# Kernel tuning notes

Hardware: AMD Instinct MI355X
Metric: run time of the kernel (lower is better)

## Reference

```python
import jax, jax.numpy as jnp
import numpy as np

EMB = 768
HEADS = 12
HD = EMB // HEADS          # 64
WS = 14                    # window size
MLP = 4 * EMB
SCALE = HD ** -0.5

# relative-position lookup indices (q_size == k_size == WS)
_REL_IDX = np.arange(WS)[:, None] - np.arange(WS)[None, :] + (WS - 1)  # (WS, WS)


def setup_inputs() -> dict:
    key = jax.random.key(0)
    ks = jax.random.split(key, 12)
    w = lambda k, shape: jax.random.normal(k, shape, jnp.float32) * 0.02
    return {
        "x": jax.random.normal(ks[0], (4, 64, 64, EMB), jnp.float32),
        "clstoken": jax.random.normal(ks[1], (4, 1, EMB), jnp.float32),
        "qkv_w": w(ks[2], (EMB, 3 * EMB)),
        "qkv_b": jnp.zeros((3 * EMB,), jnp.float32),
        "proj_w": w(ks[3], (EMB, EMB)),
        "proj_b": jnp.zeros((EMB,), jnp.float32),
        "rel_pos_h": w(ks[4], (2 * WS - 1, HD)),
        "rel_pos_w": w(ks[5], (2 * WS - 1, HD)),
        "norm1_s": jnp.ones((EMB,), jnp.float32),
        "norm1_b": jnp.zeros((EMB,), jnp.float32),
        "norm2_s": jnp.ones((EMB,), jnp.float32),
        "norm2_b": jnp.zeros((EMB,), jnp.float32),
        "fc1_w": w(ks[6], (EMB, MLP)),
        "fc1_b": jnp.zeros((MLP,), jnp.float32),
        "fc2_w": w(ks[7], (MLP, EMB)),
        "fc2_b": jnp.zeros((EMB,), jnp.float32),
    }


def _layernorm(x, s, b, eps=1e-6):
    mu = jnp.mean(x, axis=-1, keepdims=True)
    var = jnp.mean(jnp.square(x - mu), axis=-1, keepdims=True)
    return (x - mu) * jax.lax.rsqrt(var + eps) * s + b


def _attn_with_clstoken(xw, cls, qkv_w, qkv_b, proj_w, proj_b, rel_pos_h, rel_pos_w):
    # xw: (Bw, WS, WS, C), cls: (Bw, 1, C)
    Bw = xw.shape[0]
    NP = WS * WS                                   # patch tokens per window
    tokens = jnp.concatenate([cls, xw.reshape(Bw, NP, EMB)], axis=1)  # (Bw, T, C)
    T = NP + 1
    qkv = (tokens @ qkv_w + qkv_b).reshape(Bw, T, 3, HEADS, HD)
    q, k, v = [qkv[:, :, i].transpose(0, 2, 1, 3) for i in range(3)]  # (Bw, H, T, HD)
    attn = jnp.einsum("bhqd,bhkd->bhqk", q * SCALE, k)                # (Bw, H, T, T)
    # decomposed relative-position bias on the patch-patch sub-block
    Rh = rel_pos_h[_REL_IDX]                       # (WS, WS, HD)
    Rw = rel_pos_w[_REL_IDX]
    r_q = q[:, :, 1:, :].reshape(Bw, HEADS, WS, WS, HD)
    rel_h = jnp.einsum("bnhwc,hkc->bnhwk", r_q, Rh)  # (Bw, H, WS, WS, WS)
    rel_w = jnp.einsum("bnhwc,wkc->bnhwk", r_q, Rw)
    bias = (rel_h[..., :, None] + rel_w[..., None, :]).reshape(Bw, HEADS, NP, NP)
    attn = attn.at[:, :, 1:, 1:].add(bias)
    attn = jax.nn.softmax(attn, axis=-1)
    out = jnp.einsum("bhqk,bhkd->bhqd", attn, v)
    out = out.transpose(0, 2, 1, 3).reshape(Bw, T, EMB) @ proj_w + proj_b
    return out[:, 1:, :].reshape(Bw, WS, WS, EMB), out[:, :1, :]


def reference(x, clstoken, qkv_w, qkv_b, proj_w, proj_b, rel_pos_h, rel_pos_w,
              norm1_s, norm1_b, norm2_s, norm2_b, fc1_w, fc1_b, fc2_w, fc2_b):
    B, H, W, C = x.shape
    HW = H * W
    tokens = jnp.concatenate([clstoken, x.reshape(B, HW, C)], axis=1)
    shortcut = tokens
    t = _layernorm(tokens, norm1_s, norm1_b)
    cls_n = t[:, :1, :]
    xn = t[:, 1:, :].reshape(B, H, W, C)
    # window partition with padding
    pad_h = (WS - H % WS) % WS
    pad_w = (WS - W % WS) % WS
    Hp, Wp = H + pad_h, W + pad_w
    xp = jnp.pad(xn, ((0, 0), (0, pad_h), (0, pad_w), (0, 0)))
    nH, nW = Hp // WS, Wp // WS
    n_windows = nH * nW
    xw = xp.reshape(B, nH, WS, nW, WS, C).transpose(0, 1, 3, 2, 4, 5)
    xw = xw.reshape(B * n_windows, WS, WS, C)
    cls_w = jnp.repeat(cls_n, n_windows, axis=0)   # repeat_interleave over batch dim
    xw, cls_w = _attn_with_clstoken(xw, cls_w, qkv_w, qkv_b, proj_w, proj_b,
                                    rel_pos_h, rel_pos_w)
    # window unpartition
    xu = xw.reshape(B, nH, nW, WS, WS, C).transpose(0, 1, 3, 2, 4, 5)
    xu = xu.reshape(B, Hp, Wp, C)[:, :H, :W, :]
    cls_out = cls_w.reshape(B, n_windows, 1, C).mean(axis=1)
    y = jnp.concatenate([cls_out, xu.reshape(B, HW, C)], axis=1)
    tokens = shortcut + y
    h = _layernorm(tokens, norm2_s, norm2_b)
    tokens = tokens + (jax.nn.gelu(h @ fc1_w + fc1_b) @ fc2_w + fc2_b)
    return tokens  # (B, 1 + H*W, C)
```

## Files before the change

kernel.cpp:

```cpp
#include <hip/hip_runtime.h>
#include <hip/hip_bf16.h>

typedef __hip_bfloat16 bf;
typedef __bf16 bf16x8 __attribute__((ext_vector_type(8)));
typedef float f32x4 __attribute__((ext_vector_type(4)));
typedef unsigned short u16x4 __attribute__((ext_vector_type(4)));

#define DEVI __device__ __forceinline__

DEVI float b2f(bf v){ return __bfloat162float(v); }

DEVI float bfbits(unsigned short v){
  unsigned u = (unsigned)v << 16; float f; __builtin_memcpy(&f, &u, 4); return f;
}

DEVI float ldx(const void* p, size_t i, int f){
  return f ? __bfloat162float(((const bf*)p)[i]) : ((const float*)p)[i];
}

DEVI f32x4 mfma16(bf16x8 a, bf16x8 b, f32x4 c){
  return __builtin_amdgcn_mfma_f32_16x16x32_bf16(a, b, c, 0, 0, 0);
}

DEVI float gelu_t(float x){
  float u = 0.7978845608028654f * (x + 0.044715f * x * x * x);
  u = fminf(fmaxf(u, -30.f), 30.f);
  float e = __expf(2.f * u);
  return 0.5f * x * (1.f + (e - 1.f) / (e + 1.f));
}

DEVI void gload16(const bf* g, char* l){
  __builtin_amdgcn_global_load_lds((const __attribute__((address_space(1))) void*)g,
                                   (__attribute__((address_space(3))) void*)l, 16, 0, 0);
}

__global__ void detect_dtype(const void* n1s, int* flag){
  unsigned u = *(const unsigned*)n1s;
  *flag = (u == 0x3F800000u) ? 0 : 1;
}

__global__ __launch_bounds__(256) void conv_bf16(const void* src, bf* dst, int n, const int* flag){
  int f = *flag;
  int i = blockIdx.x * 256 + threadIdx.x;
  if (i < n) dst[i] = f ? ((const bf*)src)[i] : __float2bfloat16(((const float*)src)[i]);
}

__global__ __launch_bounds__(256) void transpose_w(const void* __restrict__ W, bf* __restrict__ Wt,
                                                   int K, int N, const int* flag){
  __shared__ bf tile[32][33];
  const int f = *flag;
  int n0 = blockIdx.x * 32, k0 = blockIdx.y * 32;
  int tx = threadIdx.x & 31, ty = threadIdx.x >> 5;
  #pragma unroll
  for (int i = ty; i < 32; i += 8)
    tile[i][tx] = __float2bfloat16(ldx(W, (size_t)(k0 + i) * N + n0 + tx, f));
  __syncthreads();
  #pragma unroll
  for (int i = ty; i < 32; i += 8) Wt[(size_t)(n0 + i) * K + k0 + tx] = tile[tx][i];
}

DEVI void blockreduce2(float& s, float& s2){
  #pragma unroll
  for (int off = 32; off > 0; off >>= 1){
    s  += __shfl_down(s, off);
    s2 += __shfl_down(s2, off);
  }
  __shared__ float sh[8];
  int wv = threadIdx.x >> 6;
  if ((threadIdx.x & 63) == 0){ sh[wv*2] = s; sh[wv*2+1] = s2; }
  __syncthreads();
  s  = sh[0] + sh[2] + sh[4] + sh[6];
  s2 = sh[1] + sh[3] + sh[5] + sh[7];
}

__global__ __launch_bounds__(256) void ln_window(const void* __restrict__ x, const void* __restrict__ cls,
    const bf* __restrict__ g, const bf* __restrict__ bb, bf* __restrict__ winx, int b0,
    const int* flag){
  const int f = *flag;
  int row = blockIdx.x;
  int wid_g = row / 197, p = row % 197;
  int batch = b0 + wid_g / 25;
  int wid = wid_g % 25;
  int wi = wid / 5, wj = wid % 5;
  bf* dst = winx + (size_t)row * 768;
  int tid = threadIdx.x;
  const void* src = nullptr;
  size_t base = 0;
  if (p == 0){ src = cls; base = (size_t)batch * 768; }
  else {
    int pi = (p - 1) / 14, pj = (p - 1) % 14;
    int gh = wi * 14 + pi, gw = wj * 14 + pj;
    if (gh < 64 && gw < 64){ src = x; base = ((size_t)((batch * 64 + gh) * 64 + gw)) * 768; }
  }
  if (!src){
    for (int c = tid; c < 768; c += 256) dst[c] = __float2bfloat16(0.f);
    return;
  }
  float v[3]; float s = 0.f, s2 = 0.f;
  #pragma unroll
  for (int k = 0; k < 3; k++){ v[k] = ldx(src, base + tid + k*256, f); s += v[k]; s2 += v[k]*v[k]; }
  blockreduce2(s, s2);
  float mu  = s  * (1.f/768.f);
  float var = fmaxf(s2 * (1.f/768.f) - mu*mu, 0.f);
  float rs  = rsqrtf(var + 1e-6f);
  #pragma unroll
  for (int k = 0; k < 3; k++){
    int c = tid + k*256;
    dst[c] = __float2bfloat16((v[k]-mu)*rs*b2f(g[c]) + b2f(bb[c]));
  }
}

__global__ __launch_bounds__(256) void ln_f32(const float* __restrict__ in, const bf* __restrict__ g,
    const bf* __restrict__ bb, bf* __restrict__ outb){
  size_t row = blockIdx.x;
  const float* src = in + row * 768;
  bf* dst = outb + row * 768;
  int tid = threadIdx.x;
  float v[3]; float s = 0.f, s2 = 0.f;
  #pragma unroll
  for (int k = 0; k < 3; k++){ v[k] = src[tid + k*256]; s += v[k]; s2 += v[k]*v[k]; }
  blockreduce2(s, s2);
  float mu  = s  * (1.f/768.f);
  float var = fmaxf(s2 * (1.f/768.f) - mu*mu, 0.f);
  float rs  = rsqrtf(var + 1e-6f);
  #pragma unroll
  for (int k = 0; k < 3; k++){
    int c = tid + k*256;
    dst[c] = __float2bfloat16((v[k]-mu)*rs*b2f(g[c]) + b2f(bb[c]));
  }
}

__global__ __launch_bounds__(512) void gemm128(const bf* __restrict__ A, const bf* __restrict__ Bt,
    const bf* __restrict__ bias, const float* __restrict__ res, void* __restrict__ out,
    int M, int N, int K, int flags, const int* dflag, int row_off)
{
  __shared__ __bf16 sA[2][128*64];
  __shared__ __bf16 sB[2][128*64];
  const int df = *dflag;
  const int gx = gridDim.x;
  const int nwg = gx * gridDim.y;
  const int lin = blockIdx.y * gx + blockIdx.x;
  const int q = nwg >> 3, r = nwg & 7;
  const int xcd = lin & 7, pos = lin >> 3;
  const int logical = (xcd < r ? xcd * (q + 1) : r * (q + 1) + (xcd - r) * q) + pos;
  const int m0 = (logical / gx) * 128, n0 = (logical % gx) * 128;

  const int tid = threadIdx.x, wv = tid >> 6, l = tid & 63;
  const int wm = (wv >> 2) * 64;
  const int wn = (wv & 3) * 32;
  const int li = l & 15, lk = l >> 4;
  const int xr = li & 7;

  f32x4 acc[4][2];
  #pragma unroll
  for (int i = 0; i < 4; i++)
    #pragma unroll
    for (int j = 0; j < 2; j++){ f32x4 z = {0.f,0.f,0.f,0.f}; acc[i][j] = z; }

  const int rA = tid >> 3;
  const int sl = (tid & 7) ^ (rA & 7);
  const bf* gA0 = A  + (size_t)(m0 + rA)      * K + sl * 8;
  const bf* gA1 = A  + (size_t)(m0 + 64 + rA) * K + sl * 8;
  const bf* gB0 = Bt + (size_t)(n0 + rA)      * K + sl * 8;
  const bf* gB1 = Bt + (size_t)(n0 + 64 + rA) * K + sl * 8;
  const int ldsbase = wv * 1024;

  const int nt = K >> 6;
  {
    gload16(gA0, (char*)sA[0] + ldsbase);
    gload16(gA1, (char*)sA[0] + 8192 + ldsbase);
    gload16(gB0, (char*)sB[0] + ldsbase);
    gload16(gB1, (char*)sB[0] + 8192 + ldsbase);
  }
  asm volatile("s_waitcnt vmcnt(0)" ::: "memory");
  __syncthreads();

  int cur = 0;
  for (int t = 0; t < nt; t++){
    if (t + 1 < nt){
      const int ke = (t + 1) << 6;
      gload16(gA0 + ke, (char*)sA[cur^1] + ldsbase);
      gload16(gA1 + ke, (char*)sA[cur^1] + 8192 + ldsbase);
      gload16(gB0 + ke, (char*)sB[cur^1] + ldsbase);
      gload16(gB1 + ke, (char*)sB[cur^1] + 8192 + ldsbase);
    }
    const __bf16* cA = sA[cur];
    const __bf16* cB = sB[cur];
    #pragma unroll
    for (int ks = 0; ks < 2; ks++){
      const int so = ((ks*4 + lk) ^ xr) * 8;
      bf16x8 af[4], bfr[2];
      #pragma unroll
      for (int i = 0; i < 4; i++) af[i]  = *(const bf16x8*)&cA[(wm + i*16 + li)*64 + so];
      #pragma unroll
      for (int j = 0; j < 2; j++) bfr[j] = *(const bf16x8*)&cB[(wn + j*16 + li)*64 + so];
      #pragma unroll
      for (int i = 0; i < 4; i++)
        #pragma unroll
        for (int j = 0; j < 2; j++) acc[i][j] = mfma16(af[i], bfr[j], acc[i][j]);
    }
    asm volatile("s_waitcnt vmcnt(0)" ::: "memory");
    __syncthreads();
    cur ^= 1;
  }

  #pragma unroll
  for (int i = 0; i < 4; i++){
    #pragma unroll
    for (int j = 0; j < 2; j++){
      int colg = n0 + wn + j*16 + li;
      float bc = b2f(bias[colg]);
      #pragma unroll
      for (int r2 = 0; r2 < 4; r2++){
        int rowg = m0 + wm + i*16 + lk*4 + r2;
        if (rowg < M){
          float vv = acc[i][j][r2] + bc;
          if (flags & 1) vv = gelu_t(vv);
          if (flags & 2) vv += res[(size_t)rowg * N + colg];
          if (flags & 4){
            size_t oidx = (size_t)(row_off + rowg) * N + colg;
            if (df == 0) ((float*)out)[oidx] = vv;
            else         ((bf*)out)[oidx]    = __float2bfloat16(vv);
          } else {
            ((bf*)out)[(size_t)rowg * N + colg] = __float2bfloat16(vv);
          }
        }
      }
    }
  }
}

__global__ __launch_bounds__(256) void bias_tables(const bf* __restrict__ qkv,
    const bf* __restrict__ rph, const bf* __restrict__ rpw, bf* __restrict__ relT){
  const int blk = blockIdx.x;
  const int w = blk / 12, h = blk % 12;
  const int tid = threadIdx.x, wv = tid >> 6, l = tid & 63;
  const int li = l & 15, lk = l >> 4;
  const bf* qbase = qkv + (size_t)w * 197 * 2304 + h * 64;
  bf* tbase = relT + (size_t)blk * 5600;
  for (int g = wv; g < 28; g += 4){
    bool isH = (g < 14);
    int pfix = isH ? g : (g - 14);
    int var  = li < 13 ? li : 13;
    int q = isH ? (1 + pfix*14 + var) : (1 + var*14 + pfix);
    f32x4 acc = {0.f,0.f,0.f,0.f};
    const bf* rp = isH ? rph : rpw;
    #pragma unroll
    for (int s = 0; s < 2; s++){
      bf16x8 a = *(const bf16x8*)(qbase + (size_t)q * 2304 + s*32 + lk*8);
      int idx = pfix + 13 - li;
      if (idx < 0) idx = 0;
      bf16x8 b = *(const bf16x8*)(rp + idx * 64 + s*32 + lk*8);
      acc = mfma16(a, b, acc);
    }
    #pragma unroll
    for (int r = 0; r < 4; r++){
      int mrow = lk*4 + r;
      int col = li;
      if (mrow <= 13 && col <= 13){
        int qi = isH ? (pfix*14 + mrow) : (mrow*14 + pfix);
        tbase[(isH ? 0 : 2800) + col*200 + qi + 1] = __float2bfloat16(acc[r]);
      }
    }
  }
}

__global__ __launch_bounds__(256) void attn_win(const bf* __restrict__ qkv,
    const bf* __restrict__ relT, bf* __restrict__ aout){
  __shared__ __bf16 Vt[64][232];
  __shared__ __bf16 Pl[4][16][232];
  const int blk = blockIdx.x;
  const int wh = blk >> 1, half = blk & 1;
  const int w = wh / 12, h = wh % 12;
  const int tid = threadIdx.x, wv = tid >> 6, l = tid & 63;
  const int li = l & 15, lk = l >> 4;
  const bf* qp = qkv + (size_t)w * 197 * 2304 + h * 64;
  const bf* kp = qp + 768;
  const bf* vp = qp + 1536;
  {
    const int cc = (tid & 7) * 8, rb = tid >> 3;
    #pragma unroll
    for (int pass = 0; pass < 7; pass++){
      int r = pass * 32 + rb;
      __bf16 vvv[8];
      if (r < 197){
        bf16x8 t = *(const bf16x8*)(vp + (size_t)r * 2304 + cc);
        #pragma unroll
        for (int e = 0; e < 8; e++) vvv[e] = t[e];
      } else {
        #pragma unroll
        for (int e = 0; e < 8; e++) vvv[e] = (__bf16)0.f;
      }
      #pragma unroll
      for (int e = 0; e < 8; e++) Vt[cc + e][r] = vvv[e];
    }
  }
  for (int i = l; i < 256; i += 64) Pl[wv][i >> 4][208 + (i & 15)] = (__bf16)0.f;
  __syncthreads();
  const bf* rHT = relT + (size_t)wh * 5600;
  const bf* rWT = rHT + 2800;
  const int qt0 = half * 7;
  const int nqt = half ? 6 : 7;
  for (int qt_l = wv; qt_l < nqt; qt_l += 4){
    const int qt = qt0 + qt_l;
    const int grow0 = qt*16 + lk*4;
    int qrow = qt * 16 + li; if (qrow > 196) qrow = 196;
    bf16x8 qa0 = *(const bf16x8*)(qp + (size_t)qrow * 2304 + lk*8);
    bf16x8 qa1 = *(const bf16x8*)(qp + (size_t)qrow * 2304 + 32 + lk*8);
    f32x4 sc[13];
    #pragma unroll
    for (int ct = 0; ct < 13; ct++){
      int kr = ct * 16 + li; if (kr > 196) kr = 196;
      bf16x8 kb0 = *(const bf16x8*)(kp + (size_t)kr * 2304 + lk*8);
      bf16x8 kb1 = *(const bf16x8*)(kp + (size_t)kr * 2304 + 32 + lk*8);
      f32x4 z = {0.f,0.f,0.f,0.f};
      z = mfma16(qa0, kb0, z);
      z = mfma16(qa1, kb1, z);
      sc[ct] = z;
    }
    float mx[4] = {-3e38f, -3e38f, -3e38f, -3e38f};
    #pragma unroll
    for (int ct = 0; ct < 13; ct++){
      const int col = ct * 16 + li;
      const int kiq = col >= 1 ? col - 1 : 0;
      const int kh = (kiq * 4682) >> 16;
      const int kw = kiq - kh * 14;
      const u16x4 rh4 = *(const u16x4*)(rHT + kh*200 + grow0);
      const u16x4 rw4 = *(const u16x4*)(rWT + kw*200 + grow0);
      #pragma unroll
      for (int r = 0; r < 4; r++){
        int grow = grow0 + r;
        float s = sc[ct][r] * 0.125f;
        if (col >= 197) s = -1e30f;
        else if (col >= 1 && grow >= 1 && grow < 197)
          s += bfbits(rh4[r]) + bfbits(rw4[r]);
        sc[ct][r] = s;
        mx[r] = fmaxf(mx[r], s);
      }
    }
    #pragma unroll
    for (int r = 0; r < 4; r++){
      #pragma unroll
      for (int off = 1; off < 16; off <<= 1) mx[r] = fmaxf(mx[r], __shfl_xor(mx[r], off));
    }
    float den[4] = {0.f,0.f,0.f,0.f};
    #pragma unroll
    for (int ct = 0; ct < 13; ct++)
      #pragma unroll
      for (int r = 0; r < 4; r++){
        float e = __expf(sc[ct][r] - mx[r]);
        sc[ct][r] = e; den[r] += e;
      }
    #pragma unroll
    for (int r = 0; r < 4; r++){
      #pragma unroll
      for (int off = 1; off < 16; off <<= 1) den[r] += __shfl_xor(den[r], off);
      den[r] = 1.f / den[r];
    }
    #pragma unroll
    for (int ct = 0; ct < 13; ct++)
      #pragma unroll
      for (int r = 0; r < 4; r++)
        Pl[wv][lk*4 + r][ct*16 + li] = (__bf16)(sc[ct][r] * den[r]);
    asm volatile("s_waitcnt lgkmcnt(0)" ::: "memory");
    __builtin_amdgcn_sched_barrier(0);
    #pragma unroll
    for (int n = 0; n < 4; n++){
      f32x4 o = {0.f,0.f,0.f,0.f};
      #pragma unroll
      for (int ks = 0; ks < 7; ks++){
        bf16x8 pa = *(const bf16x8*)&Pl[wv][li][ks*32 + lk*8];
        bf16x8 vb = *(const bf16x8*)&Vt[n*16 + li][ks*32 + lk*8];
        o = mfma16(pa, vb, o);
      }
      #pragma unroll
      for (int r = 0; r < 4; r++){
        int grow = qt * 16 + lk*4 + r;
        if (grow < 197)
          aout[((size_t)w * 197 + grow) * 768 + h*64 + n*16 + li] = __float2bfloat16(o[r]);
      }
    }
  }
}

__global__ __launch_bounds__(256) void unwindow(const void* __restrict__ x, const void* __restrict__ cls,
    const bf* __restrict__ projoC, float* __restrict__ tok2, int b0, const int* flag){
  const int f = *flag;
  int tg = blockIdx.x;
  int bl = tg / 4097, t = tg % 4097;
  int batch = b0 + bl;
  const bf* projo = projoC + (size_t)bl * 4925 * 768;
  for (int c = threadIdx.x; c < 768; c += 256){
    float val, add;
    if (t == 0){
      val = ldx(cls, (size_t)batch * 768 + c, f);
      float s = 0.f;
      #pragma unroll
      for (int wi = 0; wi < 25; wi++)
        s += b2f(projo[((size_t)wi * 197) * 768 + c]);
      add = s * 0.04f;
    } else {
      int idx = t - 1, gh = idx >> 6, gw = idx & 63;
      int wi = gh / 14, pi = gh % 14, wj = gw / 14, pj = gw % 14;
      int wwin = wi*5 + wj, tl = 1 + pi*14 + pj;
      val = ldx(x, ((size_t)batch * 4096 + idx) * 768 + c, f);
      add = b2f(projo[((size_t)wwin * 197 + tl) * 768 + c]);
    }
    tok2[((size_t)batch * 4097 + t) * 768 + c] = val + add;
  }
}

extern "C" void kernel_launch(void* const* d_in, const int* in_sizes, int n_in,
                              void* d_out, int out_size, void* d_ws, size_t ws_size,
                              hipStream_t stream){
  (void)in_sizes; (void)n_in; (void)out_size;
  const void* x      = d_in[0];
  const void* cls    = d_in[1];
  const void* qkv_w  = d_in[2];
  const void* qkv_bv = d_in[3];
  const void* proj_w = d_in[4];
  const void* proj_bv= d_in[5];
  const void* rph    = d_in[6];
  const void* rpw    = d_in[7];
  const void* n1s    = d_in[8];
  const void* n1b    = d_in[9];
  const void* n2s    = d_in[10];
  const void* n2b    = d_in[11];
  const void* fc1_w  = d_in[12];
  const void* fc1_bv = d_in[13];
  const void* fc2_w  = d_in[14];
  const void* fc2_bv = d_in[15];

  char* ws = (char*)d_ws;
  int* flagp  = (int*)(ws + 0);
  bf* wt_qkv  = (bf*)(ws + 256);
  bf* wt_proj = (bf*)(ws + 3539200);
  bf* wt_fc1  = (bf*)(ws + 4718848);
  bf* wt_fc2  = (bf*)(ws + 9437440);
  bf* c_qkv_b = (bf*)(ws + 14156032);
  bf* c_proj_b= (bf*)(ws + 14160640);
  bf* c_fc1_b = (bf*)(ws + 14162176);
  bf* c_fc2_b = (bf*)(ws + 14168320);
  bf* c_n1s   = (bf*)(ws + 14169856);
  bf* c_n1b   = (bf*)(ws + 14171392);
  bf* c_n2s   = (bf*)(ws + 14172928);
  bf* c_n2b   = (bf*)(ws + 14174464);
  bf* c_rph   = (bf*)(ws + 14176000);
  bf* c_rpw   = (bf*)(ws + 14179456);

  const size_t base0 = 14188800;
  int nb = 1;
  if      (ws_size >= base0 + 4ull*37824000 + 50343936) nb = 4;
  else if (ws_size >= base0 + 2ull*37824000 + 50343936) nb = 2;
  const size_t o_winx  = base0;
  const size_t o_qkv   = o_winx + (size_t)nb * 7564800;
  const size_t o_projo = o_qkv  + (size_t)nb * 22694400;
  const size_t o_tok2  = o_projo+ (size_t)nb * 7564800;
  const size_t o_fc1g  = base0  + (size_t)nb * 6292992;

  bf* winx_c  = (bf*)(ws + o_winx);
  bf* attn_oC = winx_c;
  bf* qkvC    = (bf*)(ws + o_qkv);
  bf* projoC  = (bf*)(ws + o_projo);
  bf* relT    = (bf*)(ws + o_projo);
  float* tok2 = (float*)(ws + o_tok2);
  bf* hbufC   = (bf*)(ws + base0);
  bf* fc1gC   = (bf*)(ws + o_fc1g);

  detect_dtype<<<1, 1, 0, stream>>>(n1s, flagp);

  conv_bf16<<<9,  256, 0, stream>>>(qkv_bv,  c_qkv_b, 2304, flagp);
  conv_bf16<<<3,  256, 0, stream>>>(proj_bv, c_proj_b, 768, flagp);
  conv_bf16<<<12, 256, 0, stream>>>(fc1_bv,  c_fc1_b, 3072, flagp);
  conv_bf16<<<3,  256, 0, stream>>>(fc2_bv,  c_fc2_b,  768, flagp);
  conv_bf16<<<3,  256, 0, stream>>>(n1s, c_n1s, 768, flagp);
  conv_bf16<<<3,  256, 0, stream>>>(n1b, c_n1b, 768, flagp);
  conv_bf16<<<3,  256, 0, stream>>>(n2s, c_n2s, 768, flagp);
  conv_bf16<<<3,  256, 0, stream>>>(n2b, c_n2b, 768, flagp);
  conv_bf16<<<7,  256, 0, stream>>>(rph, c_rph, 1728, flagp);
  conv_bf16<<<7,  256, 0, stream>>>(rpw, c_rpw, 1728, flagp);

  transpose_w<<<dim3(72, 24), 256, 0, stream>>>(qkv_w, wt_qkv, 768, 2304, flagp);
  transpose_w<<<dim3(24, 24), 256, 0, stream>>>(proj_w, wt_proj, 768, 768, flagp);
  transpose_w<<<dim3(96, 24), 256, 0, stream>>>(fc1_w, wt_fc1, 768, 3072, flagp);
  transpose_w<<<dim3(24, 96), 256, 0, stream>>>(fc2_w, wt_fc2, 3072, 768, flagp);

  const int nchunk = 4 / nb;
  for (int ci = 0; ci < nchunk; ci++){
    const int b0 = ci * nb;
    const int Mq = nb * 4925;
    const int gy = (Mq + 127) / 128;
    ln_window<<<nb*4925, 256, 0, stream>>>(x, cls, c_n1s, c_n1b, winx_c, b0, flagp);
    gemm128<<<dim3(18, gy), 512, 0, stream>>>(winx_c, wt_qkv, c_qkv_b, nullptr, qkvC,
                                              Mq, 2304, 768, 0, flagp, 0);
    bias_tables<<<nb*300, 256, 0, stream>>>(qkvC, c_rph, c_rpw, relT);
    attn_win<<<nb*600, 256, 0, stream>>>(qkvC, relT, attn_oC);
    gemm128<<<dim3(6, gy), 512, 0, stream>>>(attn_oC, wt_proj, c_proj_b, nullptr, projoC,
                                             Mq, 768, 768, 0, flagp, 0);
    unwindow<<<nb*4097, 256, 0, stream>>>(x, cls, projoC, tok2, b0, flagp);
  }

  for (int ci = 0; ci < nchunk; ci++){
    const int b0 = ci * nb;
    const int Mm = nb * 4097;
    const int gym = (Mm + 127) / 128;
    ln_f32<<<Mm, 256, 0, stream>>>(tok2 + (size_t)b0 * 4097 * 768, c_n2s, c_n2b, hbufC);
    gemm128<<<dim3(24, gym), 512, 0, stream>>>(hbufC, wt_fc1, c_fc1_b, nullptr, fc1gC,
                                               Mm, 3072, 768, 1, flagp, 0);
    gemm128<<<dim3(6, gym), 512, 0, stream>>>(fc1gC, wt_fc2, c_fc2_b,
                                              tok2 + (size_t)b0 * 4097 * 768,
                                              d_out,
                                              Mm, 768, 3072, 2 | 4, flagp, b0 * 4097);
  }
}
```

Baseline: 710.4 us.

## Restructure window attention: transposed scores, register-shuffled P operand, LDS-staged bias

The bias tables are re-laid out per query row (stride 18) and bulk-copied into LDS with global_load_lds, so the bias add reads from LDS instead of strided global loads. The QK^T MFMA operands are swapped, so each lane holds one query column. The softmax reductions then need only two cross-lane shuffles, and the probability tile is built into the PV MFMA A-operand through register shuffles rather than an LDS round trip. The V transpose in LDS gets an XOR swizzle to reduce bank conflicts. The kernel now handles a whole window-head per 512-thread block instead of two 256-thread half blocks. That changes occupancy and leaves waves unevenly loaded, since 13 query tiles are spread over 8 waves.

```diff
diff --git a/kernel.cpp b/kernel.cpp
--- a/kernel.cpp
+++ b/kernel.cpp
@@ -4,15 +4,11 @@
 typedef __hip_bfloat16 bf;
 typedef __bf16 bf16x8 __attribute__((ext_vector_type(8)));
 typedef float f32x4 __attribute__((ext_vector_type(4)));
-typedef unsigned short u16x4 __attribute__((ext_vector_type(4)));
+typedef int i32x4 __attribute__((ext_vector_type(4)));
 
 #define DEVI __device__ __forceinline__
 
 DEVI float b2f(bf v){ return __bfloat162float(v); }
-
-DEVI float bfbits(unsigned short v){
-  unsigned u = (unsigned)v << 16; float f; __builtin_memcpy(&f, &u, 4); return f;
-}
 
 DEVI float ldx(const void* p, size_t i, int f){
   return f ? __bfloat162float(((const bf*)p)[i]) : ((const float*)p)[i];
@@ -27,6 +23,13 @@
   u = fminf(fmaxf(u, -30.f), 30.f);
   float e = __expf(2.f * u);
   return 0.5f * x * (1.f + (e - 1.f) / (e + 1.f));
+}
+
+DEVI unsigned pk2(float a, float b){
+  bf x = __float2bfloat16(a), y = __float2bfloat16(b);
+  unsigned short ux, uy;
+  __builtin_memcpy(&ux, &x, 2); __builtin_memcpy(&uy, &y, 2);
+  return (unsigned)ux | ((unsigned)uy << 16);
 }
 
 DEVI void gload16(const bf* g, char* l){
@@ -237,7 +240,7 @@
   const int tid = threadIdx.x, wv = tid >> 6, l = tid & 63;
   const int li = l & 15, lk = l >> 4;
   const bf* qbase = qkv + (size_t)w * 197 * 2304 + h * 64;
-  bf* tbase = relT + (size_t)blk * 5600;
+  bf* tbase = relT + (size_t)blk * 7056;
   for (int g = wv; g < 28; g += 4){
     bool isH = (g < 14);
     int pfix = isH ? g : (g - 14);
@@ -259,52 +262,58 @@
       int col = li;
       if (mrow <= 13 && col <= 13){
         int qi = isH ? (pfix*14 + mrow) : (mrow*14 + pfix);
-        tbase[(isH ? 0 : 2800) + col*200 + qi + 1] = __float2bfloat16(acc[r]);
-      }
-    }
-  }
-}
-
-__global__ __launch_bounds__(256) void attn_win(const bf* __restrict__ qkv,
+        tbase[(isH ? 0 : 3528) + qi*18 + col] = __float2bfloat16(acc[r]);
+      }
+    }
+  }
+}
+
+__global__ __launch_bounds__(512, 4) void attn_win(const bf* __restrict__ qkv,
     const bf* __restrict__ relT, bf* __restrict__ aout){
-  __shared__ __bf16 Vt[64][232];
-  __shared__ __bf16 Pl[4][16][232];
+  __shared__ __bf16 VtL[64*232];
+  __shared__ __bf16 relL[8192];
   const int blk = blockIdx.x;
-  const int wh = blk >> 1, half = blk & 1;
-  const int w = wh / 12, h = wh % 12;
+  const int w = blk / 12, h = blk % 12;
   const int tid = threadIdx.x, wv = tid >> 6, l = tid & 63;
   const int li = l & 15, lk = l >> 4;
   const bf* qp = qkv + (size_t)w * 197 * 2304 + h * 64;
   const bf* kp = qp + 768;
   const bf* vp = qp + 1536;
+
+  {
+    const bf* tbase = relT + (size_t)blk * 7056;
+    gload16(tbase + (size_t)tid * 8,        (char*)relL + wv * 1024);
+    gload16(tbase + 4096 + (size_t)tid * 8, (char*)relL + 8192 + wv * 1024);
+  }
   {
     const int cc = (tid & 7) * 8, rb = tid >> 3;
-    #pragma unroll
-    for (int pass = 0; pass < 7; pass++){
-      int r = pass * 32 + rb;
-      __bf16 vvv[8];
-      if (r < 197){
-        bf16x8 t = *(const bf16x8*)(vp + (size_t)r * 2304 + cc);
+    const int xw = (tid & 7) << 3;
+    #pragma unroll
+    for (int pass = 0; pass < 4; pass++){
+      int r = pass * 64 + rb;
+      if (r < 224){
+        __bf16 vvv[8];
+        if (r < 197){
+          bf16x8 t = *(const bf16x8*)(vp + (size_t)r * 2304 + cc);
+          #pragma unroll
+          for (int e = 0; e < 8; e++) vvv[e] = t[e];
+        } else {
+          #pragma unroll
+          for (int e = 0; e < 8; e++) vvv[e] = (__bf16)0.f;
+        }
         #pragma unroll
-        for (int e = 0; e < 8; e++) vvv[e] = t[e];
-      } else {
-        #pragma unroll
-        for (int e = 0; e < 8; e++) vvv[e] = (__bf16)0.f;
-      }
-      #pragma unroll
-      for (int e = 0; e < 8; e++) Vt[cc + e][r] = vvv[e];
-    }
-  }
-  for (int i = l; i < 256; i += 64) Pl[wv][i >> 4][208 + (i & 15)] = (__bf16)0.f;
+        for (int e = 0; e < 8; e++)
+          VtL[(((cc + e) * 232 + r) ^ xw)] = vvv[e];
+      }
+    }
+  }
+  asm volatile("s_waitcnt vmcnt(0)" ::: "memory");
   __syncthreads();
-  const bf* rHT = relT + (size_t)wh * 5600;
-  const bf* rWT = rHT + 2800;
-  const int qt0 = half * 7;
-  const int nqt = half ? 6 : 7;
-  for (int qt_l = wv; qt_l < nqt; qt_l += 4){
-    const int qt = qt0 + qt_l;
-    const int grow0 = qt*16 + lk*4;
-    int qrow = qt * 16 + li; if (qrow > 196) qrow = 196;
+
+  const int qg = 0;  (void)qg;
+  for (int qt = wv; qt < 13; qt += 8){
+    const int myq = qt * 16 + li;
+    int qrow = myq > 196 ? 196 : myq;
     bf16x8 qa0 = *(const bf16x8*)(qp + (size_t)qrow * 2304 + lk*8);
     bf16x8 qa1 = *(const bf16x8*)(qp + (size_t)qrow * 2304 + 32 + lk*8);
     f32x4 sc[13];
@@ -314,70 +323,90 @@
       bf16x8 kb0 = *(const bf16x8*)(kp + (size_t)kr * 2304 + lk*8);
       bf16x8 kb1 = *(const bf16x8*)(kp + (size_t)kr * 2304 + 32 + lk*8);
       f32x4 z = {0.f,0.f,0.f,0.f};
-      z = mfma16(qa0, kb0, z);
-      z = mfma16(qa1, kb1, z);
+      z = mfma16(kb0, qa0, z);
+      z = mfma16(kb1, qa1, z);
       sc[ct] = z;
     }
-    float mx[4] = {-3e38f, -3e38f, -3e38f, -3e38f};
+    const bool qok = (myq >= 1 && myq < 197);
+    const int qi18 = (myq - 1) * 18;
+    float mx = -3e38f;
     #pragma unroll
     for (int ct = 0; ct < 13; ct++){
-      const int col = ct * 16 + li;
-      const int kiq = col >= 1 ? col - 1 : 0;
-      const int kh = (kiq * 4682) >> 16;
-      const int kw = kiq - kh * 14;
-      const u16x4 rh4 = *(const u16x4*)(rHT + kh*200 + grow0);
-      const u16x4 rw4 = *(const u16x4*)(rWT + kw*200 + grow0);
       #pragma unroll
       for (int r = 0; r < 4; r++){
-        int grow = grow0 + r;
+        int key = ct*16 + lk*4 + r;
         float s = sc[ct][r] * 0.125f;
-        if (col >= 197) s = -1e30f;
-        else if (col >= 1 && grow >= 1 && grow < 197)
-          s += bfbits(rh4[r]) + bfbits(rw4[r]);
+        if (key >= 197) s = -1e30f;
+        else if (key >= 1 && qok){
+          int ki = key - 1;
+          int kh = (ki * 4682) >> 16;
+          int kw = ki - kh * 14;
+          s += b2f(*(const bf*)&relL[qi18 + kh]) + b2f(*(const bf*)&relL[3528 + qi18 + kw]);
+        }
         sc[ct][r] = s;
-        mx[r] = fmaxf(mx[r], s);
-      }
-    }
-    #pragma unroll
-    for (int r = 0; r < 4; r++){
-      #pragma unroll
-      for (int off = 1; off < 16; off <<= 1) mx[r] = fmaxf(mx[r], __shfl_xor(mx[r], off));
-    }
-    float den[4] = {0.f,0.f,0.f,0.f};
+        mx = fmaxf(mx, s);
+      }
+    }
+    mx = fmaxf(mx, __shfl_xor(mx, 16));
+    mx = fmaxf(mx, __shfl_xor(mx, 32));
+    float den = 0.f;
     #pragma unroll
     for (int ct = 0; ct < 13; ct++)
       #pragma unroll
       for (int r = 0; r < 4; r++){
-        float e = __expf(sc[ct][r] - mx[r]);
-        sc[ct][r] = e; den[r] += e;
-      }
-    #pragma unroll
-    for (int r = 0; r < 4; r++){
-      #pragma unroll
-      for (int off = 1; off < 16; off <<= 1) den[r] += __shfl_xor(den[r], off);
-      den[r] = 1.f / den[r];
-    }
-    #pragma unroll
-    for (int ct = 0; ct < 13; ct++)
-      #pragma unroll
-      for (int r = 0; r < 4; r++)
-        Pl[wv][lk*4 + r][ct*16 + li] = (__bf16)(sc[ct][r] * den[r]);
-    asm volatile("s_waitcnt lgkmcnt(0)" ::: "memory");
-    __builtin_amdgcn_sched_barrier(0);
+        float e = __expf(sc[ct][r] - mx);
+        sc[ct][r] = e; den += e;
+      }
+    den += __shfl_xor(den, 16);
+    den += __shfl_xor(den, 32);
+    float rden = 1.f / den;
+    unsigned pw0[13], pw1[13];
+    #pragma unroll
+    for (int ct = 0; ct < 13; ct++){
+      pw0[ct] = pk2(sc[ct][0]*rden, sc[ct][1]*rden);
+      pw1[ct] = pk2(sc[ct][2]*rden, sc[ct][3]*rden);
+    }
+    const int selhi = (lk >> 1) & 1;
+    const int srcA = li + ((lk & 1) << 5);
+    const int srcB = srcA + 16;
+    f32x4 o[4];
+    #pragma unroll
+    for (int n = 0; n < 4; n++){ f32x4 z = {0.f,0.f,0.f,0.f}; o[n] = z; }
+    #pragma unroll
+    for (int wn32 = 0; wn32 < 7; wn32++){
+      const int t0 = 2*wn32, t1 = 2*wn32 + 1;
+      unsigned s0a = __shfl(pw0[t0], srcA);
+      unsigned s1a = __shfl(pw1[t0], srcA);
+      unsigned s0b = __shfl(pw0[t0], srcB);
+      unsigned s1b = __shfl(pw1[t0], srcB);
+      unsigned u0a = 0, u1a = 0, u0b = 0, u1b = 0;
+      if (t1 < 13){
+        u0a = __shfl(pw0[t1], srcA);
+        u1a = __shfl(pw1[t1], srcA);
+        u0b = __shfl(pw0[t1], srcB);
+        u1b = __shfl(pw1[t1], srcB);
+      }
+      i32x4 aw;
+      aw[0] = (int)(selhi ? u0a : s0a);
+      aw[1] = (int)(selhi ? u1a : s1a);
+      aw[2] = (int)(selhi ? u0b : s0b);
+      aw[3] = (int)(selhi ? u1b : s1b);
+      bf16x8 af = *(bf16x8*)&aw;
+      #pragma unroll
+      for (int n = 0; n < 4; n++){
+        int dim = n*16 + li;
+        int bidx = (dim*232 + wn32*32 + lk*8) ^ (((dim >> 3) & 7) << 3);
+        bf16x8 vb = *(const bf16x8*)&VtL[bidx];
+        o[n] = mfma16(af, vb, o[n]);
+      }
+    }
     #pragma unroll
     for (int n = 0; n < 4; n++){
-      f32x4 o = {0.f,0.f,0.f,0.f};
-      #pragma unroll
-      for (int ks = 0; ks < 7; ks++){
-        bf16x8 pa = *(const bf16x8*)&Pl[wv][li][ks*32 + lk*8];
-        bf16x8 vb = *(const bf16x8*)&Vt[n*16 + li][ks*32 + lk*8];
-        o = mfma16(pa, vb, o);
-      }
       #pragma unroll
       for (int r = 0; r < 4; r++){
-        int grow = qt * 16 + lk*4 + r;
+        int grow = qt*16 + lk*4 + r;
         if (grow < 197)
-          aout[((size_t)w * 197 + grow) * 768 + h*64 + n*16 + li] = __float2bfloat16(o[r]);
+          aout[((size_t)w * 197 + grow) * 768 + h*64 + n*16 + li] = __float2bfloat16(o[n][r]);
       }
     }
   }
@@ -494,7 +523,7 @@
     gemm128<<<dim3(18, gy), 512, 0, stream>>>(winx_c, wt_qkv, c_qkv_b, nullptr, qkvC,
                                               Mq, 2304, 768, 0, flagp, 0);
     bias_tables<<<nb*300, 256, 0, stream>>>(qkvC, c_rph, c_rpw, relT);
-    attn_win<<<nb*600, 256, 0, stream>>>(qkvC, relT, attn_oC);
+    attn_win<<<nb*300, 512, 0, stream>>>(qkvC, relT, attn_oC);
     gemm128<<<dim3(6, gy), 512, 0, stream>>>(attn_oC, wt_proj, c_proj_b, nullptr, projoC,
                                              Mq, 768, 768, 0, flagp, 0);
     unwindow<<<nb*4097, 256, 0, stream>>>(x, cls, projoC, tok2, b0, flagp);
```

After: 971.8 us. 36.8% more time.
